# Performance work log

Measured on AMD Instinct MI355X. Metric: run time of the kernel, lower is better.

The kernel has to match this reference:

```python
import jax, jax.numpy as jnp
import numpy as np

EMBED_DIM = 1024
NUM_HEADS = 16
HEAD_DIM = EMBED_DIM // NUM_HEADS
SCALING = HEAD_DIM ** -0.5
T, B = 1024, 4


def setup_inputs() -> dict:
    key = jax.random.key(0)
    k1, k2, k3, k4 = jax.random.split(key, 4)
    x_TBC = jax.random.normal(k1, (T, B, EMBED_DIM), dtype=jnp.float32)
    key_padding_mask = jnp.zeros((B, T), dtype=bool)
    edge_bias = jax.random.normal(k2, (B, NUM_HEADS, T, T), dtype=jnp.float32)
    # xavier_uniform-ish init for weights
    lim_qkv = (6.0 / (EMBED_DIM + 3 * EMBED_DIM)) ** 0.5 / (2 ** 0.5)
    w_qkv = jax.random.uniform(k3, (3 * EMBED_DIM, EMBED_DIM), minval=-lim_qkv, maxval=lim_qkv, dtype=jnp.float32)
    b_qkv = jnp.zeros((3 * EMBED_DIM,), dtype=jnp.float32)
    lim_p = (6.0 / (2 * EMBED_DIM)) ** 0.5
    w_proj = jax.random.uniform(k4, (EMBED_DIM, EMBED_DIM), minval=-lim_p, maxval=lim_p, dtype=jnp.float32)
    b_proj = jnp.zeros((EMBED_DIM,), dtype=jnp.float32)
    return {"x_TBC": x_TBC, "key_padding_mask": key_padding_mask, "edge_bias": edge_bias,
            "w_qkv": w_qkv, "b_qkv": b_qkv, "w_proj": w_proj, "b_proj": b_proj}


def reference(x_TBC, key_padding_mask, edge_bias, w_qkv, b_qkv, w_proj, b_proj):
    Tn, Bn, C = x_TBC.shape
    H, Dh = NUM_HEADS, HEAD_DIM
    qkv = x_TBC @ w_qkv.T + b_qkv               # [T,B,3C]
    q, k, v = jnp.split(qkv, 3, axis=-1)
    def split_heads(t):  # [T,B,C] -> [B,H,T,Dh]
        return t.reshape(Tn, Bn, H, Dh).transpose(1, 2, 0, 3)
    q = split_heads(q) * SCALING
    k = split_heads(k)
    v = split_heads(v)
    logits = jnp.einsum('bhtd,bhsd->bhts', q, k) + edge_bias  # [B,H,T,T]
    neg_inf = jnp.finfo(logits.dtype).min
    logits = jnp.where(key_padding_mask[:, None, None, :], neg_inf, logits)
    attn = jax.nn.softmax(logits, axis=-1)
    out = jnp.einsum('bhts,bhsd->bhtd', attn, v)  # [B,H,T,Dh]
    out = out.transpose(2, 0, 1, 3).reshape(Tn, Bn, C)  # [T,B,C]
    out = out @ w_proj.T + b_proj
    return out
```

## Files before the change

kernel.cpp:

```cpp
#include <hip/hip_runtime.h>
#include <stdint.h>
#include <math.h>

#define TT  1024
#define BBN 4
#define CCH 1024
#define HHN 16
#define DHD 64
#define MMR 4096
#define N3  3072

typedef __attribute__((ext_vector_type(4))) float  f32x4;
typedef __attribute__((ext_vector_type(8))) short  s16x8;
typedef __attribute__((ext_vector_type(8))) __bf16 bf16x8;

static __device__ __forceinline__ f32x4 mfma16(s16x8 a, s16x8 b, f32x4 c) {
  return __builtin_amdgcn_mfma_f32_16x16x32_bf16(
      __builtin_bit_cast(bf16x8, a), __builtin_bit_cast(bf16x8, b), c, 0, 0, 0);
}

static __device__ __forceinline__ unsigned short f2bf(float f) {
  union { float f; unsigned int u; } v; v.f = f;
  unsigned int u = v.u;
  return (unsigned short)((u + 0x7FFFu + ((u >> 16) & 1u)) >> 16);
}

typedef const __attribute__((address_space(1))) void GVoid;
typedef __attribute__((address_space(3))) void LVoid;
static __device__ __forceinline__ void gll16(const void* g, void* l) {
  __builtin_amdgcn_global_load_lds((GVoid*)g, (LVoid*)l, 16, 0, 0);
}

#if __has_builtin(__builtin_amdgcn_exp2f)
#define EXP2F(x) __builtin_amdgcn_exp2f(x)
#else
#define EXP2F(x) exp2f(x)
#endif

__global__ void cvt_all(const float* __restrict__ x, const float* __restrict__ wqkv,
                        const float* __restrict__ wproj, unsigned short* __restrict__ out) {
  int i = blockIdx.x * blockDim.x + threadIdx.x;
  const float4* src;
  int off;
  if (i < 1048576)      { src = (const float4*)x;     off = 0; }
  else if (i < 1835008) { src = (const float4*)wqkv;  off = 1048576; }
  else                  { src = (const float4*)wproj; off = 1835008; }
  float4 f = src[i - off];
  ushort4 o;
  o.x = f2bf(f.x); o.y = f2bf(f.y); o.z = f2bf(f.z); o.w = f2bf(f.w);
  ((ushort4*)out)[i] = o;
}

template <int MODE>
__global__ __launch_bounds__(256, 2) void gemm_bt(
    const unsigned short* __restrict__ A, const unsigned short* __restrict__ Bw,
    const float* __restrict__ bias, float* __restrict__ Cout,
    unsigned short* __restrict__ qb, unsigned short* __restrict__ kb,
    unsigned short* __restrict__ vtb, int M, int N, int K) {
  __shared__ __align__(16) unsigned short sA[128 * 64];
  __shared__ __align__(16) unsigned short sB[128 * 64];
  const int tid = threadIdx.x;
  const int l = tid & 63, w = tid >> 6;
  const int g = l >> 4, c = l & 15;
  const int wr = w >> 1, wc = w & 1;
  const int total = gridDim.x * gridDim.y;
  const int flat = blockIdx.y * gridDim.x + blockIdx.x;
  const int wg = (flat & 7) * (total >> 3) + (flat >> 3);
  const int bxs = wg % gridDim.x, bys = wg / gridDim.x;
  const int bm = bys * 128, bn = bxs * 128;
  const int srow = tid >> 3, sch = tid & 7;

  const unsigned short* Agp = A + (size_t)(bm + srow) * K + sch * 8;
  const unsigned short* Bgp = Bw + (size_t)(bn + srow) * K + sch * 8;
  unsigned short* sAw = &sA[w * 512];
  unsigned short* sBw = &sB[w * 512];

  f32x4 acc[4][4] = {};

  for (int k0 = 0; k0 < K; k0 += 64) {
#pragma unroll
    for (int i = 0; i < 4; ++i) {
      gll16(Agp + (size_t)i * 32 * K + k0, sAw + i * 2048);
      gll16(Bgp + (size_t)i * 32 * K + k0, sBw + i * 2048);
    }
    __syncthreads();
#pragma unroll
    for (int kk2 = 0; kk2 < 2; ++kk2) {
      s16x8 af[4], bfr[4];
#pragma unroll
      for (int mi = 0; mi < 4; ++mi)
        af[mi] = *(const s16x8*)&sA[(wr * 64 + mi * 16 + c) * 64 + kk2 * 32 + g * 8];
#pragma unroll
      for (int ni = 0; ni < 4; ++ni)
        bfr[ni] = *(const s16x8*)&sB[(wc * 64 + ni * 16 + c) * 64 + kk2 * 32 + g * 8];
#pragma unroll
      for (int mi = 0; mi < 4; ++mi)
#pragma unroll
        for (int ni = 0; ni < 4; ++ni)
          acc[mi][ni] = mfma16(af[mi], bfr[ni], acc[mi][ni]);
    }
    __syncthreads();
  }

#pragma unroll
  for (int mi = 0; mi < 4; ++mi)
#pragma unroll
    for (int ni = 0; ni < 4; ++ni) {
      const int col = bn + wc * 64 + ni * 16 + c;
      const float bsv = bias[col];
      if (MODE == 0) {
#pragma unroll
        for (int j = 0; j < 4; ++j) {
          const int r = bm + wr * 64 + mi * 16 + g * 4 + j;
          Cout[(size_t)r * N + col] = acc[mi][ni][j] + bsv;
        }
      } else {
        const int part = col >> 10;
        const int rem = col & 1023;
        const int h = rem >> 6, d = rem & 63;
        const float qscale = 0.18033688f;
#pragma unroll
        for (int j = 0; j < 4; ++j) {
          const int r = bm + wr * 64 + mi * 16 + g * 4 + j;
          const int t = r >> 2, bb = r & 3;
          const int bh = bb * 16 + h;
          float av = acc[mi][ni][j] + bsv;
          if (part == 0)      qb[((size_t)bh * 1024 + t) * 64 + d] = f2bf(av * qscale);
          else if (part == 1) kb[((size_t)bh * 1024 + t) * 64 + d] = f2bf(av);
          else                vtb[((size_t)bh * 64 + d) * 1024 + t] = f2bf(av);
        }
      }
    }
}

__global__ __launch_bounds__(256, 3) void attn_kernel(
    const unsigned short* __restrict__ qb, const unsigned short* __restrict__ kb,
    const unsigned short* __restrict__ vtb, const float* __restrict__ eb,
    const unsigned char* __restrict__ mask, unsigned short* __restrict__ ob) {
  __shared__ __align__(16) unsigned short sQ[64 * 64];
  __shared__ __align__(16) unsigned short sK[2][64 * 64];
  __shared__ __align__(16) unsigned short sV[2][64 * 64];
  __shared__ __align__(16) unsigned short sP[4][16 * 72];
  const int tid = threadIdx.x;
  const int l = tid & 63, w = tid >> 6;
  const int g = l >> 4, c = l & 15;
  const int flat = blockIdx.y * 16 + blockIdx.x;
  const int wg = (flat & 7) * 128 + (flat >> 3);
  const int q0 = (wg & 15) * 64;
  const int bh = wg >> 4;
  const int b = bh >> 4;
  const int srow = tid >> 3, sch = tid & 7;

  const unsigned short* qg = qb + (size_t)bh * 65536;
  const unsigned short* kg = kb + (size_t)bh * 65536;
  const unsigned short* vg = vtb + (size_t)bh * 65536;
  const float* ebg = eb + (size_t)bh * 1048576 + (size_t)(q0 + w * 16 + g * 4) * 1024;

  const float BS = 1.44269504f;
  float ps[4] = {0.f, 0.f, 0.f, 0.f};
  f32x4 po[4] = {};
  float bvA[4][4], bvB[4][4], mkA[4], mkB[4];

#define STAGE_KV(t, p) do {                                                      \
    int ss_ = (t) * 64;                                                          \
    _Pragma("unroll")                                                            \
    for (int i_ = 0; i_ < 2; ++i_) {                                             \
      int row_ = i_ * 32 + srow;                                                 \
      gll16(kg + (size_t)(ss_ + row_) * 64 + (sch ^ (row_ & 7)) * 8,             \
            &sK[p][i_ * 2048 + w * 512]);                                        \
      gll16(vg + (size_t)row_ * 1024 + ss_ + (sch ^ (row_ & 7)) * 8,             \
            &sV[p][i_ * 2048 + w * 512]);                                        \
    } } while (0)

#define LOAD_BIAS(t, bv, mk) do {                                                \
    int ss_ = (t) * 64;                                                          \
    _Pragma("unroll")                                                            \
    for (int ni_ = 0; ni_ < 4; ++ni_) {                                          \
      _Pragma("unroll")                                                          \
      for (int j_ = 0; j_ < 4; ++j_)                                             \
        bv[ni_][j_] = ebg[(size_t)j_ * 1024 + ss_ + ni_ * 16 + c];               \
      mk[ni_] = mask[b * TT + ss_ + ni_ * 16 + c] ? -1e30f : -8.0f;              \
    } } while (0)

#define COMPUTE(p, bv, mk) do {                                                  \
                                                                  \
    s16x8 kf_[4][2];                                                             \
    _Pragma("unroll")                                                            \
    for (int ni_ = 0; ni_ < 4; ++ni_)                                            \
      _Pragma("unroll")                                                          \
      for (int k2_ = 0; k2_ < 2; ++k2_) {                                        \
        int row_ = ni_ * 16 + c;                                                 \
        kf_[ni_][k2_] = *(const s16x8*)&sK[p][row_ * 64 +                        \
                         (((k2_ * 4 + g) ^ (row_ & 7)) * 8)];                    \
      }                                                                          \
    f32x4 sc_[4] = {};                                                           \
    __builtin_amdgcn_s_setprio(1);                                               \
    _Pragma("unroll")                                                            \
    for (int k2_ = 0; k2_ < 2; ++k2_)                                            \
      _Pragma("unroll")                                                          \
      for (int ni_ = 0; ni_ < 4; ++ni_)                                          \
        sc_[ni_] = mfma16(qf[k2_], kf_[ni_][k2_], sc_[ni_]);                     \
    __builtin_amdgcn_s_setprio(0);                                               \
                 \
    _Pragma("unroll")                                                            \
    for (int ni_ = 0; ni_ < 4; ++ni_)                                            \
      _Pragma("unroll")                                                          \
      for (int j_ = 0; j_ < 4; ++j_) {                                           \
        float x_ = fmaf(bv[ni_][j_], BS, sc_[ni_][j_]) + mk[ni_];                \
        float p_ = EXP2F(x_);                                                    \
        sP[w][(g * 4 + j_) * 72 + ni_ * 16 + c] = f2bf(p_);                      \
        ps[j_] += p_;                                                            \
      }                                                                          \
                  \
    s16x8 vf_[4][2];                                                             \
    _Pragma("unroll")                                                            \
    for (int nd_ = 0; nd_ < 4; ++nd_)                                            \
      _Pragma("unroll")                                                          \
      for (int k2_ = 0; k2_ < 2; ++k2_) {                                        \
        int row_ = nd_ * 16 + c;                                                 \
        vf_[nd_][k2_] = *(const s16x8*)&sV[p][row_ * 64 +                        \
                         (((k2_ * 4 + g) ^ (row_ & 7)) * 8)];                    \
      }                                                                          \
    asm volatile("s_waitcnt lgkmcnt(0)" ::: "memory");                           \
    __builtin_amdgcn_sched_barrier(0);                                           \
    s16x8 pf_[2];                                                                \
    _Pragma("unroll")                                                            \
    for (int k2_ = 0; k2_ < 2; ++k2_)                                            \
      pf_[k2_] = *(const s16x8*)&sP[w][c * 72 + k2_ * 32 + g * 8];               \
    __builtin_amdgcn_s_setprio(1);                                               \
    _Pragma("unroll")                                                            \
    for (int k2_ = 0; k2_ < 2; ++k2_)                                            \
      _Pragma("unroll")                                                          \
      for (int nd_ = 0; nd_ < 4; ++nd_)                                          \
        po[nd_] = mfma16(pf_[k2_], vf_[nd_][k2_], po[nd_]);                      \
    __builtin_amdgcn_s_setprio(0);                                               \
  } while (0)

#pragma unroll
  for (int i = 0; i < 2; ++i) {
    int row = i * 32 + srow;
    gll16(qg + (size_t)(q0 + row) * 64 + (sch ^ (row & 7)) * 8, &sQ[i * 2048 + w * 512]);
  }
  STAGE_KV(0, 0);
  LOAD_BIAS(0, bvA, mkA);
  __syncthreads();

  s16x8 qf[2];
#pragma unroll
  for (int kk2 = 0; kk2 < 2; ++kk2) {
    int row = w * 16 + c;
    qf[kk2] = *(const s16x8*)&sQ[row * 64 + (((kk2 * 4 + g) ^ (row & 7)) * 8)];
  }

  STAGE_KV(1, 1);
  LOAD_BIAS(1, bvB, mkB);
  COMPUTE(0, bvA, mkA);
  for (int it = 1; it < 8; ++it) {
    __syncthreads();
    STAGE_KV(2 * it, 0);
    LOAD_BIAS(2 * it, bvA, mkA);
    COMPUTE(1, bvB, mkB);
    __syncthreads();
    if (2 * it + 1 < 16) {
      STAGE_KV(2 * it + 1, 1);
      LOAD_BIAS(2 * it + 1, bvB, mkB);
    }
    COMPUTE(0, bvA, mkA);
  }
  __syncthreads();
  COMPUTE(1, bvB, mkB);

#undef STAGE_KV
#undef LOAD_BIAS
#undef COMPUTE

#pragma unroll
  for (int j = 0; j < 4; ++j) {
#pragma unroll
    for (int off = 1; off <= 8; off <<= 1)
      ps[j] += __shfl_xor(ps[j], off, 64);
    ps[j] = 1.0f / ps[j];
  }

  const int h = bh & 15;
#pragma unroll
  for (int nd = 0; nd < 4; ++nd)
#pragma unroll
    for (int j = 0; j < 4; ++j) {
      float val = po[nd][j] * ps[j];
      int t = q0 + w * 16 + g * 4 + j;
      ob[((size_t)t * 4 + b) * 1024 + h * 64 + nd * 16 + c] = f2bf(val);
    }
}

extern "C" void kernel_launch(void* const* d_in, const int* in_sizes, int n_in,
                              void* d_out, int out_size, void* d_ws, size_t ws_size,
                              hipStream_t stream) {
  const float* x      = (const float*)d_in[0];
  const unsigned char* mask = (const unsigned char*)d_in[1];
  const float* ebias  = (const float*)d_in[2];
  const float* wqkv   = (const float*)d_in[3];
  const float* bqkv   = (const float*)d_in[4];
  const float* wproj  = (const float*)d_in[5];
  const float* bproj  = (const float*)d_in[6];
  float* out = (float*)d_out;

  char* ws = (char*)d_ws;
  unsigned short* xb    = (unsigned short*)(ws);
  unsigned short* wqkvb = (unsigned short*)(ws + 8388608);
  unsigned short* wpb   = (unsigned short*)(ws + 14680064);
  unsigned short* qbuf  = (unsigned short*)(ws + 16777216);
  unsigned short* kbuf  = (unsigned short*)(ws + 25165824);
  unsigned short* vtbuf = (unsigned short*)(ws + 33554432);
  unsigned short* obuf  = (unsigned short*)(ws + 41943040);

  cvt_all<<<8192, 256, 0, stream>>>(x, wqkv, wproj, xb);

  gemm_bt<1><<<dim3(24, 32), 256, 0, stream>>>(
      xb, wqkvb, bqkv, nullptr, qbuf, kbuf, vtbuf, MMR, N3, 1024);

  attn_kernel<<<dim3(16, 64), 256, 0, stream>>>(
      qbuf, kbuf, vtbuf, ebias, mask, obuf);

  gemm_bt<0><<<dim3(8, 32), 256, 0, stream>>>(
      obuf, wpb, bproj, out, nullptr, nullptr, nullptr, MMR, 1024, 1024);
}
```

Measured before the change: 164.0 us.

## Retile projection GEMM, transpose V via LDS, restructure attention pipeline

The GEMM is templated on its N tile width, and the output projection moves to 64-wide tiles so it launches more blocks. Occupancy hints are raised. The V-part epilogue of the QKV GEMM now goes through LDS so that transposed V is written with 16-byte coalesced stores instead of scattered 2-byte stores. The attention kernel caches the padding mask in LDS and prefetches two KV tiles up front. Its main loop uses raw s_barrier with explicit vmcnt waits so loads overlap compute, and the s_setprio hints are removed. The hand-counted vmcnt values are fragile and could cause races if the compiler schedules the loads differently.

```diff
diff --git a/kernel.cpp b/kernel.cpp
--- a/kernel.cpp
+++ b/kernel.cpp
@@ -51,14 +51,16 @@
   ((ushort4*)out)[i] = o;
 }
 
-template <int MODE>
-__global__ __launch_bounds__(256, 2) void gemm_bt(
+template <int MODE, int BN>
+__global__ __launch_bounds__(256, 3) void gemm_bt(
     const unsigned short* __restrict__ A, const unsigned short* __restrict__ Bw,
     const float* __restrict__ bias, float* __restrict__ Cout,
     unsigned short* __restrict__ qb, unsigned short* __restrict__ kb,
     unsigned short* __restrict__ vtb, int M, int N, int K) {
-  __shared__ __align__(16) unsigned short sA[128 * 64];
-  __shared__ __align__(16) unsigned short sB[128 * 64];
+  constexpr int NI = BN / 32;
+  __shared__ __align__(16) unsigned short sMem[128 * 64 + BN * 64];
+  unsigned short* sA = sMem;
+  unsigned short* sB = sMem + 128 * 64;
   const int tid = threadIdx.x;
   const int l = tid & 63, w = tid >> 6;
   const int g = l >> 4, c = l & 15;
@@ -67,7 +69,7 @@
   const int flat = blockIdx.y * gridDim.x + blockIdx.x;
   const int wg = (flat & 7) * (total >> 3) + (flat >> 3);
   const int bxs = wg % gridDim.x, bys = wg / gridDim.x;
-  const int bm = bys * 128, bn = bxs * 128;
+  const int bm = bys * 128, bn = bxs * BN;
   const int srow = tid >> 3, sch = tid & 7;
 
   const unsigned short* Agp = A + (size_t)(bm + srow) * K + sch * 8;
@@ -75,38 +77,73 @@
   unsigned short* sAw = &sA[w * 512];
   unsigned short* sBw = &sB[w * 512];
 
-  f32x4 acc[4][4] = {};
+  f32x4 acc[4][NI] = {};
 
   for (int k0 = 0; k0 < K; k0 += 64) {
 #pragma unroll
-    for (int i = 0; i < 4; ++i) {
+    for (int i = 0; i < 4; ++i)
       gll16(Agp + (size_t)i * 32 * K + k0, sAw + i * 2048);
+#pragma unroll
+    for (int i = 0; i < BN / 32; ++i)
       gll16(Bgp + (size_t)i * 32 * K + k0, sBw + i * 2048);
-    }
     __syncthreads();
 #pragma unroll
     for (int kk2 = 0; kk2 < 2; ++kk2) {
-      s16x8 af[4], bfr[4];
+      s16x8 af[4], bfr[NI];
 #pragma unroll
       for (int mi = 0; mi < 4; ++mi)
         af[mi] = *(const s16x8*)&sA[(wr * 64 + mi * 16 + c) * 64 + kk2 * 32 + g * 8];
 #pragma unroll
-      for (int ni = 0; ni < 4; ++ni)
-        bfr[ni] = *(const s16x8*)&sB[(wc * 64 + ni * 16 + c) * 64 + kk2 * 32 + g * 8];
+      for (int ni = 0; ni < NI; ++ni)
+        bfr[ni] = *(const s16x8*)&sB[(wc * (BN / 2) + ni * 16 + c) * 64 + kk2 * 32 + g * 8];
 #pragma unroll
       for (int mi = 0; mi < 4; ++mi)
 #pragma unroll
-        for (int ni = 0; ni < 4; ++ni)
+        for (int ni = 0; ni < NI; ++ni)
           acc[mi][ni] = mfma16(af[mi], bfr[ni], acc[mi][ni]);
     }
     __syncthreads();
   }
 
+  if (MODE == 1 && (bn >> 10) == 2) {
+    unsigned short* sT = sMem;
+    const int tl0 = bm >> 2;
+#pragma unroll
+    for (int pc = 0; pc < 2; ++pc) {
+      __syncthreads();
+      if (wc == pc) {
+#pragma unroll
+        for (int mi = 0; mi < 4; ++mi)
+#pragma unroll
+          for (int ni = 0; ni < NI; ++ni) {
+            const int col = bn + pc * 64 + ni * 16 + c;
+            const float bsv = bias[col];
+#pragma unroll
+            for (int j = 0; j < 4; ++j)
+              sT[(wr * 64 + mi * 16 + g * 4 + j) * 72 + ni * 16 + c] =
+                  f2bf(acc[mi][ni][j] + bsv);
+          }
+      }
+      __syncthreads();
+      const int h = ((bn + pc * 64) & 1023) >> 6;
+      unsigned short* vdst = vtb + ((size_t)(w * 16 + h) * 64 + l) * 1024 + tl0;
+#pragma unroll
+      for (int q8 = 0; q8 < 4; ++q8) {
+        unsigned short pk[8];
+#pragma unroll
+        for (int e = 0; e < 8; ++e)
+          pk[e] = sT[(((q8 * 8 + e) << 2) | w) * 72 + l];
+        *(s16x8*)&vdst[q8 * 8] = *(const s16x8*)pk;
+      }
+    }
+    return;
+  }
+
 #pragma unroll
   for (int mi = 0; mi < 4; ++mi)
 #pragma unroll
-    for (int ni = 0; ni < 4; ++ni) {
-      const int col = bn + wc * 64 + ni * 16 + c;
+    for (int ni = 0; ni < NI; ++ni) {
+      const int col = bn + wc * (BN / 2) + ni * 16 + c;
       const float bsv = bias[col];
       if (MODE == 0) {
 #pragma unroll
@@ -115,9 +152,9 @@
           Cout[(size_t)r * N + col] = acc[mi][ni][j] + bsv;
         }
       } else {
-        const int part = col >> 10;
         const int rem = col & 1023;
         const int h = rem >> 6, d = rem & 63;
+        const bool isq = (col >> 10) == 0;
         const float qscale = 0.18033688f;
 #pragma unroll
         for (int j = 0; j < 4; ++j) {
@@ -125,9 +162,8 @@
           const int t = r >> 2, bb = r & 3;
           const int bh = bb * 16 + h;
           float av = acc[mi][ni][j] + bsv;
-          if (part == 0)      qb[((size_t)bh * 1024 + t) * 64 + d] = f2bf(av * qscale);
-          else if (part == 1) kb[((size_t)bh * 1024 + t) * 64 + d] = f2bf(av);
-          else                vtb[((size_t)bh * 64 + d) * 1024 + t] = f2bf(av);
+          if (isq) qb[((size_t)bh * 1024 + t) * 64 + d] = f2bf(av * qscale);
+          else     kb[((size_t)bh * 1024 + t) * 64 + d] = f2bf(av);
         }
       }
     }
@@ -141,6 +177,7 @@
   __shared__ __align__(16) unsigned short sK[2][64 * 64];
   __shared__ __align__(16) unsigned short sV[2][64 * 64];
   __shared__ __align__(16) unsigned short sP[4][16 * 72];
+  __shared__ __align__(4) unsigned char sM[1024];
   const int tid = threadIdx.x;
   const int l = tid & 63, w = tid >> 6;
   const int g = l >> 4, c = l & 15;
@@ -157,68 +194,64 @@
   const float* ebg = eb + (size_t)bh * 1048576 + (size_t)(q0 + w * 16 + g * 4) * 1024;
 
   const float BS = 1.44269504f;
+  float bvA[4][4], bvB[4][4];
   float ps[4] = {0.f, 0.f, 0.f, 0.f};
   f32x4 po[4] = {};
-  float bvA[4][4], bvB[4][4], mkA[4], mkB[4];
-
-#define STAGE_KV(t, p) do {                                                      \
-    int ss_ = (t) * 64;                                                          \
+
+#define STAGE(tv, P) do {                                                        \
     _Pragma("unroll")                                                            \
     for (int i_ = 0; i_ < 2; ++i_) {                                             \
       int row_ = i_ * 32 + srow;                                                 \
-      gll16(kg + (size_t)(ss_ + row_) * 64 + (sch ^ (row_ & 7)) * 8,             \
-            &sK[p][i_ * 2048 + w * 512]);                                        \
-      gll16(vg + (size_t)row_ * 1024 + ss_ + (sch ^ (row_ & 7)) * 8,             \
-            &sV[p][i_ * 2048 + w * 512]);                                        \
+      gll16(kg + (size_t)((tv) * 64 + row_) * 64 + (sch ^ (row_ & 7)) * 8,       \
+            &sK[P][i_ * 2048 + w * 512]);                                        \
+      gll16(vg + (size_t)row_ * 1024 + (tv) * 64 + (sch ^ (row_ & 7)) * 8,       \
+            &sV[P][i_ * 2048 + w * 512]);                                        \
     } } while (0)
 
-#define LOAD_BIAS(t, bv, mk) do {                                                \
-    int ss_ = (t) * 64;                                                          \
-    _Pragma("unroll")                                                            \
-    for (int ni_ = 0; ni_ < 4; ++ni_) {                                          \
+#define BIAS(tv, BV) do {                                                        \
+    _Pragma("unroll")                                                            \
+    for (int ni_ = 0; ni_ < 4; ++ni_)                                            \
       _Pragma("unroll")                                                          \
       for (int j_ = 0; j_ < 4; ++j_)                                             \
-        bv[ni_][j_] = ebg[(size_t)j_ * 1024 + ss_ + ni_ * 16 + c];               \
-      mk[ni_] = mask[b * TT + ss_ + ni_ * 16 + c] ? -1e30f : -8.0f;              \
-    } } while (0)
-
-#define COMPUTE(p, bv, mk) do {                                                  \
-                                                                  \
+        BV[ni_][j_] = ebg[(size_t)j_ * 1024 + (tv) * 64 + ni_ * 16 + c];         \
+    } while (0)
+
+#define TILE(P, BV, s0v) do {                                                    \
+    float mkc_[4];                                                               \
+    _Pragma("unroll")                                                            \
+    for (int ni_ = 0; ni_ < 4; ++ni_)                                            \
+      mkc_[ni_] = sM[(s0v) + ni_ * 16 + c] ? -1e30f : -8.0f;                     \
     s16x8 kf_[4][2];                                                             \
     _Pragma("unroll")                                                            \
     for (int ni_ = 0; ni_ < 4; ++ni_)                                            \
       _Pragma("unroll")                                                          \
       for (int k2_ = 0; k2_ < 2; ++k2_) {                                        \
         int row_ = ni_ * 16 + c;                                                 \
-        kf_[ni_][k2_] = *(const s16x8*)&sK[p][row_ * 64 +                        \
+        kf_[ni_][k2_] = *(const s16x8*)&sK[P][row_ * 64 +                        \
                          (((k2_ * 4 + g) ^ (row_ & 7)) * 8)];                    \
       }                                                                          \
     f32x4 sc_[4] = {};                                                           \
-    __builtin_amdgcn_s_setprio(1);                                               \
     _Pragma("unroll")                                                            \
     for (int k2_ = 0; k2_ < 2; ++k2_)                                            \
       _Pragma("unroll")                                                          \
       for (int ni_ = 0; ni_ < 4; ++ni_)                                          \
         sc_[ni_] = mfma16(qf[k2_], kf_[ni_][k2_], sc_[ni_]);                     \
-    __builtin_amdgcn_s_setprio(0);                                               \
-                 \
     _Pragma("unroll")                                                            \
     for (int ni_ = 0; ni_ < 4; ++ni_)                                            \
       _Pragma("unroll")                                                          \
       for (int j_ = 0; j_ < 4; ++j_) {                                           \
-        float x_ = fmaf(bv[ni_][j_], BS, sc_[ni_][j_]) + mk[ni_];                \
+        float x_ = fmaf(BV[ni_][j_], BS, sc_[ni_][j_]) + mkc_[ni_];              \
         float p_ = EXP2F(x_);                                                    \
         sP[w][(g * 4 + j_) * 72 + ni_ * 16 + c] = f2bf(p_);                      \
         ps[j_] += p_;                                                            \
       }                                                                          \
-                  \
     s16x8 vf_[4][2];                                                             \
     _Pragma("unroll")                                                            \
     for (int nd_ = 0; nd_ < 4; ++nd_)                                            \
       _Pragma("unroll")                                                          \
       for (int k2_ = 0; k2_ < 2; ++k2_) {                                        \
         int row_ = nd_ * 16 + c;                                                 \
-        vf_[nd_][k2_] = *(const s16x8*)&sV[p][row_ * 64 +                        \
+        vf_[nd_][k2_] = *(const s16x8*)&sV[P][row_ * 64 +                        \
                          (((k2_ * 4 + g) ^ (row_ & 7)) * 8)];                    \
       }                                                                          \
     asm volatile("s_waitcnt lgkmcnt(0)" ::: "memory");                           \
@@ -227,13 +260,11 @@
     _Pragma("unroll")                                                            \
     for (int k2_ = 0; k2_ < 2; ++k2_)                                            \
       pf_[k2_] = *(const s16x8*)&sP[w][c * 72 + k2_ * 32 + g * 8];               \
-    __builtin_amdgcn_s_setprio(1);                                               \
     _Pragma("unroll")                                                            \
     for (int k2_ = 0; k2_ < 2; ++k2_)                                            \
       _Pragma("unroll")                                                          \
       for (int nd_ = 0; nd_ < 4; ++nd_)                                          \
         po[nd_] = mfma16(pf_[k2_], vf_[nd_][k2_], po[nd_]);                      \
-    __builtin_amdgcn_s_setprio(0);                                               \
   } while (0)
 
 #pragma unroll
@@ -241,8 +272,11 @@
     int row = i * 32 + srow;
     gll16(qg + (size_t)(q0 + row) * 64 + (sch ^ (row & 7)) * 8, &sQ[i * 2048 + w * 512]);
   }
-  STAGE_KV(0, 0);
-  LOAD_BIAS(0, bvA, mkA);
+  STAGE(0, 0);
+  STAGE(1, 1);
+  BIAS(0, bvA);
+  BIAS(1, bvB);
+  ((unsigned int*)sM)[tid] = ((const unsigned int*)(mask + b * TT))[tid & 255];
   __syncthreads();
 
   s16x8 qf[2];
@@ -252,27 +286,25 @@
     qf[kk2] = *(const s16x8*)&sQ[row * 64 + (((kk2 * 4 + g) ^ (row & 7)) * 8)];
   }
 
-  STAGE_KV(1, 1);
-  LOAD_BIAS(1, bvB, mkB);
-  COMPUTE(0, bvA, mkA);
-  for (int it = 1; it < 8; ++it) {
-    __syncthreads();
-    STAGE_KV(2 * it, 0);
-    LOAD_BIAS(2 * it, bvA, mkA);
-    COMPUTE(1, bvB, mkB);
-    __syncthreads();
-    if (2 * it + 1 < 16) {
-      STAGE_KV(2 * it + 1, 1);
-      LOAD_BIAS(2 * it + 1, bvB, mkB);
-    }
-    COMPUTE(0, bvA, mkA);
-  }
-  __syncthreads();
-  COMPUTE(1, bvB, mkB);
-
-#undef STAGE_KV
-#undef LOAD_BIAS
-#undef COMPUTE
+#pragma unroll 1
+  for (int t2 = 0;; t2 += 2) {
+    TILE(0, bvA, t2 * 64);
+    __builtin_amdgcn_s_barrier();
+    if (t2 + 2 < 16) { STAGE(t2 + 2, 0); BIAS(t2 + 2, bvA); }
+    if (t2 == 14) { asm volatile("s_waitcnt vmcnt(16)" ::: "memory"); }
+    else          { asm volatile("s_waitcnt vmcnt(36)" ::: "memory"); }
+    __builtin_amdgcn_s_barrier();
+    TILE(1, bvB, t2 * 64 + 64);
+    if (t2 == 14) break;
+    __builtin_amdgcn_s_barrier();
+    STAGE(t2 + 3, 1); BIAS(t2 + 3, bvB);
+    asm volatile("s_waitcnt vmcnt(36)" ::: "memory");
+    __builtin_amdgcn_s_barrier();
+  }
+
+#undef STAGE
+#undef BIAS
+#undef TILE
 
 #pragma unroll
   for (int j = 0; j < 4; ++j) {
@@ -281,7 +313,6 @@
       ps[j] += __shfl_xor(ps[j], off, 64);
     ps[j] = 1.0f / ps[j];
   }
-
   const int h = bh & 15;
 #pragma unroll
   for (int nd = 0; nd < 4; ++nd)
@@ -316,12 +347,12 @@
 
   cvt_all<<<8192, 256, 0, stream>>>(x, wqkv, wproj, xb);
 
-  gemm_bt<1><<<dim3(24, 32), 256, 0, stream>>>(
+  gemm_bt<1, 128><<<dim3(24, 32), 256, 0, stream>>>(
       xb, wqkvb, bqkv, nullptr, qbuf, kbuf, vtbuf, MMR, N3, 1024);
 
   attn_kernel<<<dim3(16, 64), 256, 0, stream>>>(
       qbuf, kbuf, vtbuf, ebias, mask, obuf);
 
-  gemm_bt<0><<<dim3(8, 32), 256, 0, stream>>>(
+  gemm_bt<0, 64><<<dim3(16, 32), 256, 0, stream>>>(
       obuf, wpb, bproj, out, nullptr, nullptr, nullptr, MMR, 1024, 1024);
 }
```

After: 151.4 us. -7.7%, faster.
